# Performance work log

Hardware: AMD Instinct MI355X
Metric: run time of the kernel (lower is better)

## Reference

```python
import jax, jax.numpy as jnp
import numpy as np

N_REGS, BIT_WIDTH, KEY_DIM, B = 32, 64, 256, 262144


def _ln(x, g, b):
    m = x.mean(-1, keepdims=True)
    v = x.var(-1, keepdims=True)
    return (x - m) / jnp.sqrt(v + 1e-5) * g + b


def _gelu(x):
    return jax.nn.gelu(x, approximate=False)  # torch nn.GELU default = exact erf


def _l2norm(x):
    return x / jnp.maximum(jnp.linalg.norm(x, axis=-1, keepdims=True), 1e-12)


def _attention(idx, register_keys, temperature,
               qw1, qb1, qg1, qbt1, qw2, qb2, qg2, qbt2, qw3, qb3):
    # 5-bit binary encoding of the register index (little-endian, like the torch loop)
    bits = ((idx[:, None] >> jnp.arange(5)) & 1).astype(jnp.float32)  # (B,5)
    h = _gelu(_ln(bits @ qw1 + qb1, qg1, qbt1))                       # (B,128)
    h = _gelu(_ln(h @ qw2 + qb2, qg2, qbt2))                          # (B,256)
    q = h @ qw3 + qb3                                                 # (B,key_dim)
    sim = _l2norm(q) @ _l2norm(register_keys).T                       # (B,n_regs)
    temp = jnp.maximum(jnp.abs(temperature), 0.01)
    return jax.nn.softmax(sim / temp, axis=-1)


def setup_inputs() -> dict:
    key = jax.random.key(0)
    ks = jax.random.split(key, 10)

    def nrm(k, shape, scale=1.0):
        return jax.random.normal(k, shape, dtype=jnp.float32) * scale

    register_values = nrm(ks[0], (N_REGS, BIT_WIDTH), 0.1)
    q, _ = jnp.linalg.qr(nrm(ks[1], (KEY_DIM, N_REGS)))
    register_keys = q.T  # orthonormal rows, like nn.init.orthogonal_

    return dict(
        write_idx=jax.random.randint(ks[2], (B,), 0, 32),
        write_value=nrm(ks[3], (B, BIT_WIDTH)),
        read_idx=jax.random.randint(ks[4], (B,), 0, 32),
        register_values=register_values,
        register_keys=register_keys,
        qw1=nrm(ks[5], (5, 128), 0.3), qb1=jnp.zeros(128, jnp.float32),
        qg1=jnp.ones(128, jnp.float32), qbt1=jnp.zeros(128, jnp.float32),
        qw2=nrm(ks[6], (128, 256), 0.05), qb2=jnp.zeros(256, jnp.float32),
        qg2=jnp.ones(256, jnp.float32), qbt2=jnp.zeros(256, jnp.float32),
        qw3=nrm(ks[7], (256, KEY_DIM), 0.05), qb3=jnp.zeros(KEY_DIM, jnp.float32),
        vw1=nrm(ks[8], (BIT_WIDTH, 2 * BIT_WIDTH), 0.08), vb1=jnp.zeros(2 * BIT_WIDTH, jnp.float32),
        vg1=jnp.ones(2 * BIT_WIDTH, jnp.float32), vbt1=jnp.zeros(2 * BIT_WIDTH, jnp.float32),
        vw2=nrm(ks[9], (2 * BIT_WIDTH, BIT_WIDTH), 0.08), vb2=jnp.zeros(BIT_WIDTH, jnp.float32),
        temperature=jnp.array(1.0, jnp.float32),
        write_strength=jnp.array(1.0, jnp.float32),
    )


def reference(write_idx, write_value, read_idx, register_values, register_keys,
              qw1, qb1, qg1, qbt1, qw2, qb2, qg2, qbt2, qw3, qb3,
              vw1, vb1, vg1, vbt1, vw2, vb2, temperature, write_strength):
    qp = (qw1, qb1, qg1, qbt1, qw2, qb2, qg2, qbt2, qw3, qb3)
    n = write_value.shape[0]

    # ---- differentiable write ----
    is_xzr_w = (write_idx == 31).astype(jnp.float32)[:, None]
    val = write_value * (1.0 - is_xzr_w)
    att_w = _attention(write_idx, register_keys, temperature, *qp)     # (B,n_regs)
    enc = _gelu(_ln(val @ vw1 + vb1, vg1, vbt1)) @ vw2 + vb2           # (B,bit_width)
    s = jax.nn.sigmoid(write_strength)
    # mean over batch of (1 - s*a) * old + s*a * enc, computed without (B,n_regs,bit_width)
    new_regs = ((1.0 - s * att_w.mean(axis=0))[:, None] * register_values
                + (s / n) * jnp.einsum('bn,bd->nd', att_w, enc))       # (n_regs,bit_width)

    # ---- read against the (detached) new register state ----
    att_r = _attention(read_idx, register_keys, temperature, *qp)
    read_value = att_r @ jax.lax.stop_gradient(new_regs)
    read_value = read_value * (1.0 - (read_idx == 31).astype(jnp.float32)[:, None])
    return (read_value, new_regs)
```

## Files before the change

kernel.cpp:

```cpp
#include <hip/hip_runtime.h>
#include <hip/hip_bf16.h>
#include <math.h>

#define B_TOTAL 262144
#define NREG 32
#define BITW 64
#define NSLICE 16
#define SLICE_STRIDE (NREG*128 + NREG)

typedef float  f32x16 __attribute__((ext_vector_type(16)));
typedef short  short8 __attribute__((ext_vector_type(8)));
typedef int    i32x4  __attribute__((ext_vector_type(4)));

union FR { i32x4 w; short8 h; };

__device__ __forceinline__ unsigned pk_bf16(float a, float b){
    unsigned r;
    asm("v_cvt_pk_bf16_f32 %0, %1, %2" : "=v"(r) : "v"(a), "v"(b));
    return r;
}

__device__ __forceinline__ float geluf(float x){
    return 0.5f * x * (1.0f + erff(x * 0.70710678118654752440f));
}

__device__ __forceinline__ float gelu_fast(float x){
    float x2 = x*x;
    float t1 = fmaf(x2, 0.044715f, 1.0f);
    float z2 = x * t1 * 1.5957691216057308f;
    float e  = __expf(z2);
    float r  = __builtin_amdgcn_rcpf(e + 1.0f);
    return x - x*r;
}

__global__ void __launch_bounds__(256, 2) k_fused(
    const float* __restrict__ wval, const int* __restrict__ widx,
    const float* __restrict__ vw1, const float* __restrict__ vb1,
    const float* __restrict__ vg1, const float* __restrict__ vbt1,
    const float* __restrict__ qw1, const float* __restrict__ qb1,
    const float* __restrict__ qg1, const float* __restrict__ qbt1,
    const float* __restrict__ qw2, const float* __restrict__ qb2,
    const float* __restrict__ qg2, const float* __restrict__ qbt2,
    const float* __restrict__ qw3, const float* __restrict__ qb3,
    const float* __restrict__ keys, const float* __restrict__ temp_p,
    float* __restrict__ att_out, float* __restrict__ hgs_g)
{
    __shared__ __align__(16) unsigned s_w1p[16*64*4];
    __shared__ float s_hgs[NREG*128];
    __shared__ float s_cnt[NREG];
    __shared__ float red8[4];
    __shared__ float h1s[128];
    __shared__ float h2s[256];
    __shared__ float qns[256];
    __shared__ float svs[32];

    const int t    = threadIdx.x;
    const int lane = t & 63;
    const int wid  = t >> 6;
    const int l31  = lane & 31;
    const int lh   = lane >> 5;

    if (blockIdx.x < 32){
        const int idx = blockIdx.x;
        auto blksum = [&](float v)->float{
            #pragma unroll
            for (int o = 32; o >= 1; o >>= 1) v += __shfl_xor(v, o, 64);
            if (lane == 0) red8[wid] = v;
            __syncthreads();
            float r = red8[0] + red8[1] + red8[2] + red8[3];
            __syncthreads();
            return r;
        };

        float a1 = 0.f;
        if (t < 128){
            a1 = qb1[t];
            #pragma unroll
            for (int k = 0; k < 5; ++k)
                a1 += (float)((idx >> k) & 1) * qw1[k*128 + t];
        }
        float m1 = blksum(t < 128 ? a1 : 0.f) * (1.f/128.f);
        float d1 = (t < 128) ? (a1 - m1) : 0.f;
        float v1 = blksum(d1*d1) * (1.f/128.f);
        if (t < 128) h1s[t] = geluf(d1 * rsqrtf(v1 + 1e-5f) * qg1[t] + qbt1[t]);
        __syncthreads();

        float a2 = qb2[t];
        for (int k = 0; k < 128; ++k) a2 += h1s[k] * qw2[k*256 + t];
        float m2 = blksum(a2) * (1.f/256.f);
        float d2 = a2 - m2;
        float v2 = blksum(d2*d2) * (1.f/256.f);
        h2s[t] = geluf(d2 * rsqrtf(v2 + 1e-5f) * qg2[t] + qbt2[t]);
        __syncthreads();

        float a3 = qb3[t];
        for (int k = 0; k < 256; ++k) a3 += h2s[k] * qw3[k*256 + t];
        float nrm = blksum(a3*a3);
        qns[t] = a3 / fmaxf(sqrtf(nrm), 1e-12f);
        __syncthreads();

        if (t < 32){
            const float* kr = keys + t * 256;
            float dot = 0.f, ss = 0.f;
            for (int k = 0; k < 256; ++k){ float kv = kr[k]; dot += qns[k]*kv; ss += kv*kv; }
            svs[t] = dot / fmaxf(sqrtf(ss), 1e-12f);
        }
        __syncthreads();
        if (t < 32){
            float temp = fmaxf(fabsf(temp_p[0]), 0.01f);
            float inv = 1.f / temp;
            float mx = -1e30f;
            for (int i = 0; i < 32; ++i) mx = fmaxf(mx, svs[i]);
            float se = 0.f;
            for (int i = 0; i < 32; ++i) se += expf((svs[i] - mx) * inv);
            att_out[idx*32 + t] = expf((svs[t] - mx) * inv) / se;
        }
        return;
    }

    const int eb = blockIdx.x - 32;

    for (int e = t; e < 16*64*4; e += 256){
        int wd  = e & 3;
        int lam = (e >> 2) & 63;
        int f   = e >> 8;
        int ks  = f >> 2, jt = f & 3;
        int k0  = ks*16 + (lam >> 5)*8 + wd*2;
        int j   = jt*32 + (lam & 31);
        s_w1p[e] = pk_bf16(vw1[k0*128 + j], vw1[(k0+1)*128 + j]);
    }
    for (int e = t; e < NREG*128; e += 256) s_hgs[e] = 0.f;
    if (t < NREG) s_cnt[t] = 0.f;
    __syncthreads();

    float b1v[4], gv[4], btv[4];
    #pragma unroll
    for (int jt = 0; jt < 4; ++jt){
        b1v[jt] = vb1 [jt*32 + l31];
        gv [jt] = vg1 [jt*32 + l31];
        btv[jt] = vbt1[jt*32 + l31];
    }
    FR ones;
    #pragma unroll
    for (int w = 0; w < 4; ++w) ones.w[w] = 0x3F803F80;

    f32x16 hgs[4], cntc;
    #pragma unroll
    for (int nt = 0; nt < 4; ++nt)
        #pragma unroll
        for (int e = 0; e < 16; ++e) hgs[nt][e] = 0.f;
    #pragma unroll
    for (int e = 0; e < 16; ++e) cntc[e] = 0.f;

    const long rowbase = (long)eb*512 + (long)wid*128;

    float4 rv[8]; int wivn;
    {
        const float* rp = wval + (size_t)(rowbase + l31)*64 + lh*8;
        #pragma unroll
        for (int ks = 0; ks < 4; ++ks){
            rv[2*ks  ] = *(const float4*)(rp + ks*16);
            rv[2*ks+1] = *(const float4*)(rp + ks*16 + 4);
        }
        wivn = widx[rowbase + l31];
    }

    #pragma unroll 1
    for (int g = 0; g < 4; ++g){
        const int cur_wiv = wivn;
        const float msk = (cur_wiv == 31) ? 0.f : 1.f;

        FR va[4];
        #pragma unroll
        for (int ks = 0; ks < 4; ++ks){
            float a0 = rv[2*ks].x*msk,  a1 = rv[2*ks].y*msk;
            float a2 = rv[2*ks].z*msk,  a3 = rv[2*ks].w*msk;
            float a4 = rv[2*ks+1].x*msk, a5 = rv[2*ks+1].y*msk;
            float a6 = rv[2*ks+1].z*msk, a7 = rv[2*ks+1].w*msk;
            va[ks].w[0] = (int)pk_bf16(a0, a1);
            va[ks].w[1] = (int)pk_bf16(a2, a3);
            va[ks].w[2] = (int)pk_bf16(a4, a5);
            va[ks].w[3] = (int)pk_bf16(a6, a7);
        }
        if (g < 3){
            const float* rp = wval + (size_t)(rowbase + (g+1)*32 + l31)*64 + lh*8;
            #pragma unroll
            for (int ks = 0; ks < 4; ++ks){
                rv[2*ks  ] = *(const float4*)(rp + ks*16);
                rv[2*ks+1] = *(const float4*)(rp + ks*16 + 4);
            }
            wivn = widx[rowbase + (g+1)*32 + l31];
        }

        f32x16 C1[4];
        #pragma unroll
        for (int jt = 0; jt < 4; ++jt)
            #pragma unroll
            for (int e = 0; e < 16; ++e) C1[jt][e] = b1v[jt];
        #pragma unroll
        for (int ks = 0; ks < 4; ++ks){
            FR bw[4];
            #pragma unroll
            for (int jt = 0; jt < 4; ++jt)
                bw[jt].w = *(const i32x4*)&s_w1p[((ks*4 + jt)*64 + lane)*4];
            #pragma unroll
            for (int jt = 0; jt < 4; ++jt)
                C1[jt] = __builtin_amdgcn_mfma_f32_32x32x16_bf16(va[ks].h, bw[jt].h, C1[jt], 0, 0, 0);
        }

        f32x16 sv, qv;
        #pragma unroll
        for (int e = 0; e < 16; ++e){
            float x0 = C1[0][e], x1 = C1[1][e], x2 = C1[2][e], x3 = C1[3][e];
            sv[e] = (x0 + x1) + (x2 + x3);
            qv[e] = fmaf(x0,x0, fmaf(x1,x1, fmaf(x2,x2, x3*x3)));
        }
        #pragma unroll
        for (int o = 1; o <= 16; o <<= 1){
            #pragma unroll
            for (int e = 0; e < 16; ++e) sv[e] += __shfl_xor(sv[e], o, 64);
            #pragma unroll
            for (int e = 0; e < 16; ++e) qv[e] += __shfl_xor(qv[e], o, 64);
        }
        f32x16 mn, rs;
        #pragma unroll
        for (int e = 0; e < 16; ++e){
            float m  = sv[e] * (1.f/128.f);
            float va_= qv[e] * (1.f/128.f) - m*m;
            mn[e] = m;
            rs[e] = rsqrtf(va_ + 1e-5f);
        }
        #pragma unroll
        for (int jt = 0; jt < 4; ++jt)
            #pragma unroll
            for (int e = 0; e < 16; ++e){
                float y = fmaf((C1[jt][e] - mn[e]) * rs[e], gv[jt], btv[jt]);
                C1[jt][e] = gelu_fast(y);
            }

        #pragma unroll
        for (int ks2 = 0; ks2 < 2; ++ks2){
            FR oh;
            #pragma unroll
            for (int w = 0; w < 4; ++w){
                int b0 = ks2*16 + lh*8 + 2*w;
                int wa = __shfl(cur_wiv, b0,     64);
                int wb = __shfl(cur_wiv, b0 + 1, 64);
                oh.w[w] = (int)((wa == l31 ? 0x3F80u : 0u) | (wb == l31 ? 0x3F800000u : 0u));
            }
            cntc = __builtin_amdgcn_mfma_f32_32x32x16_bf16(oh.h, ones.h, cntc, 0, 0, 0);
            const int rb = ks2*8;
            #pragma unroll
            for (int nt = 0; nt < 4; ++nt){
                int P0 = (int)pk_bf16(C1[nt][rb+0], C1[nt][rb+1]);
                int P1 = (int)pk_bf16(C1[nt][rb+2], C1[nt][rb+3]);
                int Q0 = (int)pk_bf16(C1[nt][rb+4], C1[nt][rb+5]);
                int Q1 = (int)pk_bf16(C1[nt][rb+6], C1[nt][rb+7]);
                int sp0 = __shfl_xor(P0, 32, 64);
                int sq0 = __shfl_xor(Q0, 32, 64);
                int sp1 = __shfl_xor(P1, 32, 64);
                int sq1 = __shfl_xor(Q1, 32, 64);
                FR bf;
                bf.w[0] = lh ? sq0 : P0;
                bf.w[1] = lh ? sq1 : P1;
                bf.w[2] = lh ? Q0  : sp0;
                bf.w[3] = lh ? Q1  : sp1;
                hgs[nt] = __builtin_amdgcn_mfma_f32_32x32x16_bf16(oh.h, bf.h, hgs[nt], 0, 0, 0);
            }
        }
    }

    #pragma unroll
    for (int nt = 0; nt < 4; ++nt)
        #pragma unroll
        for (int e = 0; e < 16; ++e){
            int m = (e & 3) + 8*(e >> 2) + 4*lh;
            atomicAdd(&s_hgs[m*128 + nt*32 + l31], hgs[nt][e]);
        }
    if (l31 == 0){
        #pragma unroll
        for (int e = 0; e < 16; ++e){
            int m = (e & 3) + 8*(e >> 2) + 4*lh;
            atomicAdd(&s_cnt[m], cntc[e]);
        }
    }
    __syncthreads();

    float* dst = hgs_g + (size_t)(eb & (NSLICE-1)) * SLICE_STRIDE;
    for (int e = t; e < NREG*128; e += 256) atomicAdd(&dst[e], s_hgs[e]);
    if (t < NREG) atomicAdd(&dst[NREG*128 + t], s_cnt[t]);
}

__global__ void __launch_bounds__(256) k_combine(
    const float* __restrict__ att, const float* __restrict__ hgs_g,
    const float* __restrict__ regv, const float* __restrict__ vw2,
    const float* __restrict__ vb2, const float* __restrict__ wstr_p,
    float* __restrict__ rv_table, float* __restrict__ out_regs)
{
    __shared__ float s_hgs[NREG*128];
    __shared__ float s_cnt[NREG];
    __shared__ float s_att[NREG*NREG];
    __shared__ float s_enc[NREG*BITW];
    __shared__ float s_am[NREG];
    __shared__ float s_nr[NREG*BITW];
    const int t = threadIdx.x;

    for (int e = t; e < NREG*128; e += 256){
        float s = 0.f;
        for (int sl = 0; sl < NSLICE; ++sl) s += hgs_g[sl*SLICE_STRIDE + e];
        s_hgs[e] = s;
    }
    if (t < NREG){
        float s = 0.f;
        for (int sl = 0; sl < NSLICE; ++sl) s += hgs_g[sl*SLICE_STRIDE + NREG*128 + t];
        s_cnt[t] = s;
    }
    for (int e = t; e < NREG*NREG; e += 256) s_att[e] = att[e];
    __syncthreads();

    {
        int d = t & 63, i0 = t >> 6;
        for (int i = i0; i < NREG; i += 4){
            float acc = s_cnt[i] * vb2[d];
            for (int j = 0; j < 128; ++j)
                acc = fmaf(s_hgs[i*128 + j], vw2[j*64 + d], acc);
            s_enc[i*64 + d] = acc;
        }
    }
    if (t < NREG){
        float s = 0.f;
        for (int i = 0; i < NREG; ++i) s += s_cnt[i] * s_att[i*NREG + t];
        s_am[t] = s * (1.f / (float)B_TOTAL);
    }
    __syncthreads();

    const float s = 1.f / (1.f + expf(-wstr_p[0]));
    for (int e = t; e < NREG*BITW; e += 256){
        int r = e >> 6, d = e & 63;
        float acc = 0.f;
        for (int i = 0; i < NREG; ++i) acc = fmaf(s_att[i*NREG + r], s_enc[i*64 + d], acc);
        float nr = (1.f - s*s_am[r]) * regv[e] + (s / (float)B_TOTAL) * acc;
        s_nr[e] = nr;
        out_regs[e] = nr;
    }
    __syncthreads();
    for (int e = t; e < NREG*BITW; e += 256){
        int i = e >> 6, d = e & 63;
        float acc = 0.f;
        for (int r = 0; r < NREG; ++r) acc = fmaf(s_att[i*NREG + r], s_nr[r*64 + d], acc);
        rv_table[e] = (i == 31) ? 0.f : acc;
    }
}

__global__ void __launch_bounds__(256) k_read(
    const int* __restrict__ ridx, const float* __restrict__ rv_table,
    float* __restrict__ out)
{
    __shared__ float s_rv[NREG*BITW];
    const int t = threadIdx.x;
    for (int e = t; e < NREG*BITW; e += 256) s_rv[e] = rv_table[e];
    __syncthreads();
    const int nq = B_TOTAL * 16;
    for (int q = blockIdx.x * 256 + t; q < nq; q += gridDim.x * 256){
        int row = q >> 4;
        int sub = (q & 15) << 2;
        int ri = ridx[row];
        *(float4*)(out + (size_t)q * 4) = *(const float4*)(&s_rv[ri*64 + sub]);
    }
}

extern "C" void kernel_launch(void* const* d_in, const int* in_sizes, int n_in,
                              void* d_out, int out_size, void* d_ws, size_t ws_size,
                              hipStream_t stream)
{
    (void)in_sizes; (void)n_in; (void)out_size; (void)ws_size;
    const int*   widx = (const int*)  d_in[0];
    const float* wval = (const float*)d_in[1];
    const int*   ridx = (const int*)  d_in[2];
    const float* regv = (const float*)d_in[3];
    const float* keys = (const float*)d_in[4];
    const float* qw1  = (const float*)d_in[5];
    const float* qb1  = (const float*)d_in[6];
    const float* qg1  = (const float*)d_in[7];
    const float* qbt1 = (const float*)d_in[8];
    const float* qw2  = (const float*)d_in[9];
    const float* qb2  = (const float*)d_in[10];
    const float* qg2  = (const float*)d_in[11];
    const float* qbt2 = (const float*)d_in[12];
    const float* qw3  = (const float*)d_in[13];
    const float* qb3  = (const float*)d_in[14];
    const float* vw1  = (const float*)d_in[15];
    const float* vb1  = (const float*)d_in[16];
    const float* vg1  = (const float*)d_in[17];
    const float* vbt1 = (const float*)d_in[18];
    const float* vw2  = (const float*)d_in[19];
    const float* vb2  = (const float*)d_in[20];
    const float* temp = (const float*)d_in[21];
    const float* wstr = (const float*)d_in[22];

    float* ws    = (float*)d_ws;
    float* att   = ws;
    float* hgs_g = ws + 1024;
    float* rvt   = ws + 1024 + NSLICE*SLICE_STRIDE;
    float* out   = (float*)d_out;

    hipMemsetAsync(hgs_g, 0, (size_t)NSLICE*SLICE_STRIDE*sizeof(float), stream);
    k_fused  <<<544, 256, 0, stream>>>(wval, widx, vw1, vb1, vg1, vbt1,
                                       qw1,qb1,qg1,qbt1,qw2,qb2,qg2,qbt2,qw3,qb3,
                                       keys, temp, att, hgs_g);
    k_combine<<<1, 256, 0, stream>>>(att, hgs_g, regv, vw2, vb2, wstr,
                                     rvt, out + (size_t)B_TOTAL*64);
    k_read   <<<2048, 256, 0, stream>>>(ridx, rvt, out);
}
```

Baseline: 312.1 us.

## Cut write-kernel register pressure and stage vw2 into shared memory in combine

The write kernel now keeps the prefetched write rows as packed bf16 words and applies the zero-register mask with a bitwise AND, so the per-element float multiplies go away and fewer registers stay live. The LayerNorm reduction is split into chunks of four rows to shorten register live ranges. The per-register count is kept as an integer in each lane instead of a separate MFMA accumulator. The combine kernel copies vw2 into shared memory and reuses that buffer for the enc and nr arrays, which adds an extra barrier and a larger shared-memory footprint.

Result: slower. 599.3 us (+92.0%).

```diff
diff --git a/kernel.cpp b/kernel.cpp
--- a/kernel.cpp
+++ b/kernel.cpp
@@ -140,57 +140,53 @@
         gv [jt] = vg1 [jt*32 + l31];
         btv[jt] = vbt1[jt*32 + l31];
     }
-    FR ones;
-    #pragma unroll
-    for (int w = 0; w < 4; ++w) ones.w[w] = 0x3F803F80;
-
-    f32x16 hgs[4], cntc;
+
+    f32x16 hgs[4];
     #pragma unroll
     for (int nt = 0; nt < 4; ++nt)
         #pragma unroll
         for (int e = 0; e < 16; ++e) hgs[nt][e] = 0.f;
-    #pragma unroll
-    for (int e = 0; e < 16; ++e) cntc[e] = 0.f;
+    int cnt_i = 0;
 
     const long rowbase = (long)eb*512 + (long)wid*128;
 
-    float4 rv[8]; int wivn;
+    unsigned pv[16]; int wiv_cur;
     {
         const float* rp = wval + (size_t)(rowbase + l31)*64 + lh*8;
         #pragma unroll
         for (int ks = 0; ks < 4; ++ks){
-            rv[2*ks  ] = *(const float4*)(rp + ks*16);
-            rv[2*ks+1] = *(const float4*)(rp + ks*16 + 4);
-        }
-        wivn = widx[rowbase + l31];
+            float4 ra = *(const float4*)(rp + ks*16);
+            float4 rb = *(const float4*)(rp + ks*16 + 4);
+            pv[4*ks+0] = pk_bf16(ra.x, ra.y);
+            pv[4*ks+1] = pk_bf16(ra.z, ra.w);
+            pv[4*ks+2] = pk_bf16(rb.x, rb.y);
+            pv[4*ks+3] = pk_bf16(rb.z, rb.w);
+        }
+        wiv_cur = widx[rowbase + l31];
     }
 
     #pragma unroll 1
     for (int g = 0; g < 4; ++g){
-        const int cur_wiv = wivn;
-        const float msk = (cur_wiv == 31) ? 0.f : 1.f;
-
-        FR va[4];
-        #pragma unroll
-        for (int ks = 0; ks < 4; ++ks){
-            float a0 = rv[2*ks].x*msk,  a1 = rv[2*ks].y*msk;
-            float a2 = rv[2*ks].z*msk,  a3 = rv[2*ks].w*msk;
-            float a4 = rv[2*ks+1].x*msk, a5 = rv[2*ks+1].y*msk;
-            float a6 = rv[2*ks+1].z*msk, a7 = rv[2*ks+1].w*msk;
-            va[ks].w[0] = (int)pk_bf16(a0, a1);
-            va[ks].w[1] = (int)pk_bf16(a2, a3);
-            va[ks].w[2] = (int)pk_bf16(a4, a5);
-            va[ks].w[3] = (int)pk_bf16(a6, a7);
-        }
+        const int cur_wiv = wiv_cur;
+        const unsigned zm = (cur_wiv == 31) ? 0u : 0xFFFFFFFFu;
+
+        float4 rf[8]; int wiv_nxt = 0;
         if (g < 3){
             const float* rp = wval + (size_t)(rowbase + (g+1)*32 + l31)*64 + lh*8;
             #pragma unroll
             for (int ks = 0; ks < 4; ++ks){
-                rv[2*ks  ] = *(const float4*)(rp + ks*16);
-                rv[2*ks+1] = *(const float4*)(rp + ks*16 + 4);
-            }
-            wivn = widx[rowbase + (g+1)*32 + l31];
-        }
+                rf[2*ks  ] = *(const float4*)(rp + ks*16);
+                rf[2*ks+1] = *(const float4*)(rp + ks*16 + 4);
+            }
+            wiv_nxt = widx[rowbase + (g+1)*32 + l31];
+        }
+
+        FR va[4];
+        #pragma unroll
+        for (int ks = 0; ks < 4; ++ks)
+            #pragma unroll
+            for (int w = 0; w < 4; ++w)
+                va[ks].w[w] = (int)(pv[4*ks+w] & zm);
 
         f32x16 C1[4];
         #pragma unroll
@@ -208,50 +204,54 @@
                 C1[jt] = __builtin_amdgcn_mfma_f32_32x32x16_bf16(va[ks].h, bw[jt].h, C1[jt], 0, 0, 0);
         }
 
-        f32x16 sv, qv;
-        #pragma unroll
-        for (int e = 0; e < 16; ++e){
-            float x0 = C1[0][e], x1 = C1[1][e], x2 = C1[2][e], x3 = C1[3][e];
-            sv[e] = (x0 + x1) + (x2 + x3);
-            qv[e] = fmaf(x0,x0, fmaf(x1,x1, fmaf(x2,x2, x3*x3)));
-        }
-        #pragma unroll
-        for (int o = 1; o <= 16; o <<= 1){
-            #pragma unroll
-            for (int e = 0; e < 16; ++e) sv[e] += __shfl_xor(sv[e], o, 64);
-            #pragma unroll
-            for (int e = 0; e < 16; ++e) qv[e] += __shfl_xor(qv[e], o, 64);
-        }
-        f32x16 mn, rs;
-        #pragma unroll
-        for (int e = 0; e < 16; ++e){
-            float m  = sv[e] * (1.f/128.f);
-            float va_= qv[e] * (1.f/128.f) - m*m;
-            mn[e] = m;
-            rs[e] = rsqrtf(va_ + 1e-5f);
-        }
-        #pragma unroll
-        for (int jt = 0; jt < 4; ++jt)
-            #pragma unroll
-            for (int e = 0; e < 16; ++e){
-                float y = fmaf((C1[jt][e] - mn[e]) * rs[e], gv[jt], btv[jt]);
-                C1[jt][e] = gelu_fast(y);
-            }
-
+        #pragma unroll
+        for (int ec = 0; ec < 4; ++ec){
+            float s4[4], q4[4];
+            #pragma unroll
+            for (int u = 0; u < 4; ++u){
+                int e = ec*4 + u;
+                float x0 = C1[0][e], x1 = C1[1][e], x2 = C1[2][e], x3 = C1[3][e];
+                s4[u] = (x0 + x1) + (x2 + x3);
+                q4[u] = fmaf(x0,x0, fmaf(x1,x1, fmaf(x2,x2, x3*x3)));
+            }
+            #pragma unroll
+            for (int o = 1; o <= 16; o <<= 1){
+                #pragma unroll
+                for (int u = 0; u < 4; ++u){
+                    s4[u] += __shfl_xor(s4[u], o, 64);
+                    q4[u] += __shfl_xor(q4[u], o, 64);
+                }
+            }
+            #pragma unroll
+            for (int u = 0; u < 4; ++u){
+                int e = ec*4 + u;
+                float m  = s4[u] * (1.f/128.f);
+                float rs = rsqrtf(q4[u] * (1.f/128.f) - m*m + 1e-5f);
+                #pragma unroll
+                for (int jt = 0; jt < 4; ++jt)
+                    C1[jt][e] = gelu_fast(fmaf((C1[jt][e] - m) * rs, gv[jt], btv[jt]));
+            }
+        }
+
+        FR oh[2];
         #pragma unroll
         for (int ks2 = 0; ks2 < 2; ++ks2){
-            FR oh;
             #pragma unroll
             for (int w = 0; w < 4; ++w){
                 int b0 = ks2*16 + lh*8 + 2*w;
                 int wa = __shfl(cur_wiv, b0,     64);
                 int wb = __shfl(cur_wiv, b0 + 1, 64);
-                oh.w[w] = (int)((wa == l31 ? 0x3F80u : 0u) | (wb == l31 ? 0x3F800000u : 0u));
-            }
-            cntc = __builtin_amdgcn_mfma_f32_32x32x16_bf16(oh.h, ones.h, cntc, 0, 0, 0);
-            const int rb = ks2*8;
-            #pragma unroll
-            for (int nt = 0; nt < 4; ++nt){
+                unsigned x = (wa == l31 ? 0x3F80u : 0u) | (wb == l31 ? 0x3F800000u : 0u);
+                oh[ks2].w[w] = (int)x;
+                cnt_i += (int)((x >> 7) & 1u) + (int)((x >> 23) & 1u);
+            }
+        }
+
+        #pragma unroll
+        for (int nt = 0; nt < 4; ++nt){
+            #pragma unroll
+            for (int ks2 = 0; ks2 < 2; ++ks2){
+                const int rb = ks2*8;
                 int P0 = (int)pk_bf16(C1[nt][rb+0], C1[nt][rb+1]);
                 int P1 = (int)pk_bf16(C1[nt][rb+2], C1[nt][rb+3]);
                 int Q0 = (int)pk_bf16(C1[nt][rb+4], C1[nt][rb+5]);
@@ -265,8 +265,19 @@
                 bf.w[1] = lh ? sq1 : P1;
                 bf.w[2] = lh ? Q0  : sp0;
                 bf.w[3] = lh ? Q1  : sp1;
-                hgs[nt] = __builtin_amdgcn_mfma_f32_32x32x16_bf16(oh.h, bf.h, hgs[nt], 0, 0, 0);
-            }
+                hgs[nt] = __builtin_amdgcn_mfma_f32_32x32x16_bf16(oh[ks2].h, bf.h, hgs[nt], 0, 0, 0);
+            }
+        }
+
+        if (g < 3){
+            #pragma unroll
+            for (int ks = 0; ks < 4; ++ks){
+                pv[4*ks+0] = pk_bf16(rf[2*ks].x,   rf[2*ks].y);
+                pv[4*ks+1] = pk_bf16(rf[2*ks].z,   rf[2*ks].w);
+                pv[4*ks+2] = pk_bf16(rf[2*ks+1].x, rf[2*ks+1].y);
+                pv[4*ks+3] = pk_bf16(rf[2*ks+1].z, rf[2*ks+1].w);
+            }
+            wiv_cur = wiv_nxt;
         }
     }
 
@@ -277,13 +288,7 @@
             int m = (e & 3) + 8*(e >> 2) + 4*lh;
             atomicAdd(&s_hgs[m*128 + nt*32 + l31], hgs[nt][e]);
         }
-    if (l31 == 0){
-        #pragma unroll
-        for (int e = 0; e < 16; ++e){
-            int m = (e & 3) + 8*(e >> 2) + 4*lh;
-            atomicAdd(&s_cnt[m], cntc[e]);
-        }
-    }
+    atomicAdd(&s_cnt[l31], (float)cnt_i);
     __syncthreads();
 
     float* dst = hgs_g + (size_t)(eb & (NSLICE-1)) * SLICE_STRIDE;
@@ -297,14 +302,14 @@
     const float* __restrict__ vb2, const float* __restrict__ wstr_p,
     float* __restrict__ rv_table, float* __restrict__ out_regs)
 {
+    __shared__ float smemA[8192];
     __shared__ float s_hgs[NREG*128];
+    __shared__ float s_att[NREG*NREG];
     __shared__ float s_cnt[NREG];
-    __shared__ float s_att[NREG*NREG];
-    __shared__ float s_enc[NREG*BITW];
     __shared__ float s_am[NREG];
-    __shared__ float s_nr[NREG*BITW];
     const int t = threadIdx.x;
 
+    for (int e = t; e < 128*64; e += 256) smemA[e] = vw2[e];
     for (int e = t; e < NREG*128; e += 256){
         float s = 0.f;
         for (int sl = 0; sl < NSLICE; ++sl) s += hgs_g[sl*SLICE_STRIDE + e];
@@ -318,14 +323,16 @@
     for (int e = t; e < NREG*NREG; e += 256) s_att[e] = att[e];
     __syncthreads();
 
-    {
-        int d = t & 63, i0 = t >> 6;
-        for (int i = i0; i < NREG; i += 4){
-            float acc = s_cnt[i] * vb2[d];
-            for (int j = 0; j < 128; ++j)
-                acc = fmaf(s_hgs[i*128 + j], vw2[j*64 + d], acc);
-            s_enc[i*64 + d] = acc;
-        }
+    const int d  = t & 63;
+    const int i0 = t >> 6;
+    float enc_r[8];
+    #pragma unroll
+    for (int m = 0; m < 8; ++m){
+        int i = i0 + 4*m;
+        float acc = s_cnt[i] * vb2[d];
+        for (int j = 0; j < 128; ++j)
+            acc = fmaf(s_hgs[i*128 + j], smemA[j*64 + d], acc);
+        enc_r[m] = acc;
     }
     if (t < NREG){
         float s = 0.f;
@@ -334,20 +341,26 @@
     }
     __syncthreads();
 
+    float* s_enc = smemA;
+    float* s_nr  = smemA + 2048;
+    #pragma unroll
+    for (int m = 0; m < 8; ++m) s_enc[(i0 + 4*m)*64 + d] = enc_r[m];
+    __syncthreads();
+
     const float s = 1.f / (1.f + expf(-wstr_p[0]));
     for (int e = t; e < NREG*BITW; e += 256){
-        int r = e >> 6, d = e & 63;
+        int r = e >> 6, dd = e & 63;
         float acc = 0.f;
-        for (int i = 0; i < NREG; ++i) acc = fmaf(s_att[i*NREG + r], s_enc[i*64 + d], acc);
+        for (int i = 0; i < NREG; ++i) acc = fmaf(s_att[i*NREG + r], s_enc[i*64 + dd], acc);
         float nr = (1.f - s*s_am[r]) * regv[e] + (s / (float)B_TOTAL) * acc;
         s_nr[e] = nr;
         out_regs[e] = nr;
     }
     __syncthreads();
     for (int e = t; e < NREG*BITW; e += 256){
-        int i = e >> 6, d = e & 63;
+        int i = e >> 6, dd = e & 63;
         float acc = 0.f;
-        for (int r = 0; r < NREG; ++r) acc = fmaf(s_att[i*NREG + r], s_nr[r*64 + d], acc);
+        for (int r = 0; r < NREG; ++r) acc = fmaf(s_att[i*NREG + r], s_nr[r*64 + dd], acc);
         rv_table[e] = (i == 31) ? 0.f : acc;
     }
 }
```
